# Kernel optimization log

Measured on AMD Instinct MI355X. Metric: run time of the kernel, lower is better.

The kernel has to match this reference:

```python
import jax, jax.numpy as jnp
import numpy as np

IN_F, OUT_F, N_TOK = 4096, 4096, 8192

def setup_inputs() -> dict:
    key = jax.random.key(0)
    k1, k2, k3 = jax.random.split(key, 3)
    x = jax.random.normal(k1, (N_TOK, IN_F), dtype=jnp.float32)
    scaler = jax.random.uniform(k2, (1,), dtype=jnp.float32)
    int8_weights = jax.random.randint(k3, (IN_F, OUT_F), -128, 128, dtype=jnp.int32)
    return {"x": x, "scaler": scaler, "int8_weights": int8_weights}

def reference(x, scaler, int8_weights):
    # dequantize int8 weights: fp_w = int8_w * scaler, then GEMM
    fp_weights = int8_weights.astype(x.dtype) * scaler  # [in, out]
    return jnp.matmul(x, fp_weights)  # [tokens, out]
```

## Files before the change

### kernel.cpp

```cpp
#include <hip/hip_runtime.h>

#define M_DIM 8192
#define N_DIM 4096
#define K_DIM 4096

typedef __attribute__((ext_vector_type(8))) __bf16 bf16x8;
typedef __attribute__((ext_vector_type(4))) float f32x4;
typedef __attribute__((ext_vector_type(8))) unsigned short u16x8;

typedef const __attribute__((address_space(1))) unsigned int gu32_t;
typedef __attribute__((address_space(3))) unsigned int lu32_t;

static __device__ __forceinline__ unsigned short f2bf(float f) {
    union { float f; unsigned int u; } v; v.f = f;
    unsigned int u = v.u;
    return (unsigned short)((u + 0x7fffu + ((u >> 16) & 1u)) >> 16);
}

__global__ __launch_bounds__(256) void cvt_x_kernel(const float* __restrict__ x,
                                                    unsigned short* __restrict__ xb) {
    size_t i = (size_t)blockIdx.x * 256 + threadIdx.x;
    const float4* x4 = (const float4*)x;
    float4 a = x4[2 * i], b = x4[2 * i + 1];
    u16x8 o;
    o[0] = f2bf(a.x); o[1] = f2bf(a.y); o[2] = f2bf(a.z); o[3] = f2bf(a.w);
    o[4] = f2bf(b.x); o[5] = f2bf(b.y); o[6] = f2bf(b.z); o[7] = f2bf(b.w);
    *(u16x8*)(xb + i * 8) = o;
}

__global__ __launch_bounds__(256) void cvt_w_kernel(const int* __restrict__ w,
                                                    unsigned short* __restrict__ wt) {
    __shared__ unsigned short t[64][72];
    int n0 = blockIdx.x * 64;
    int k0 = blockIdx.y * 64;
    int tid = threadIdx.x;
#pragma unroll
    for (int i = 0; i < 16; i++) {
        int idx = tid + i * 256;
        int r = idx >> 6, c = idx & 63;
        int v = w[(size_t)(k0 + r) * N_DIM + n0 + c];
        t[c][r] = f2bf((float)v);
    }
    __syncthreads();
#pragma unroll
    for (int i = 0; i < 2; i++) {
        int slot = tid + i * 256;
        int r = slot >> 3, c = (slot & 7) * 8;
        u16x8 o = *(const u16x8*)&t[r][c];
        *(u16x8*)&wt[(size_t)(n0 + r) * K_DIM + k0 + c] = o;
    }
}

__global__ __launch_bounds__(256) void gemm_bt_kernel(const unsigned short* __restrict__ A,
                                                      const unsigned short* __restrict__ B,
                                                      const float* __restrict__ scaler,
                                                      float* __restrict__ C) {
    __shared__ unsigned short As[128 * 32];
    __shared__ unsigned short Bs[128 * 32];

    const int tid  = threadIdx.x;
    const int m0   = blockIdx.y * 128;
    const int n0   = blockIdx.x * 128;
    const int wave = tid >> 6, lane = tid & 63;
    const int quad = lane >> 4, lr = lane & 15;
    const int wm   = wave >> 1, wn = wave & 1;

    const int q0 = tid, q1 = tid + 256;
    const unsigned short* ga0 = A + (size_t)(m0 + (q0 >> 2)) * K_DIM + (q0 & 3) * 8;
    const unsigned short* ga1 = A + (size_t)(m0 + (q1 >> 2)) * K_DIM + (q1 & 3) * 8;
    const unsigned short* gb0 = B + (size_t)(n0 + (q0 >> 2)) * K_DIM + (q0 & 3) * 8;
    const unsigned short* gb1 = B + (size_t)(n0 + (q1 >> 2)) * K_DIM + (q1 & 3) * 8;
    unsigned short* la0 = As + q0 * 8;
    unsigned short* la1 = As + q1 * 8;
    unsigned short* lb0 = Bs + q0 * 8;
    unsigned short* lb1 = Bs + q1 * 8;

    f32x4 acc[4][4];
#pragma unroll
    for (int i = 0; i < 4; i++)
#pragma unroll
        for (int j = 0; j < 4; j++) acc[i][j] = (f32x4){0.f, 0.f, 0.f, 0.f};

    const unsigned short* pa = &As[(wm * 64 + lr) * 32 + quad * 8];
    const unsigned short* pb = &Bs[(wn * 64 + lr) * 32 + quad * 8];

    for (int kt = 0; kt < K_DIM / 32; ++kt) {
        __builtin_amdgcn_global_load_lds((gu32_t*)ga0, (lu32_t*)la0, 16, 0, 0);
        __builtin_amdgcn_global_load_lds((gu32_t*)ga1, (lu32_t*)la1, 16, 0, 0);
        __builtin_amdgcn_global_load_lds((gu32_t*)gb0, (lu32_t*)lb0, 16, 0, 0);
        __builtin_amdgcn_global_load_lds((gu32_t*)gb1, (lu32_t*)lb1, 16, 0, 0);
        ga0 += 32; ga1 += 32; gb0 += 32; gb1 += 32;
        __syncthreads();

        bf16x8 af[4], bf[4];
#pragma unroll
        for (int mi = 0; mi < 4; mi++) af[mi] = *(const bf16x8*)(pa + mi * 16 * 32);
#pragma unroll
        for (int ni = 0; ni < 4; ni++) bf[ni] = *(const bf16x8*)(pb + ni * 16 * 32);

#pragma unroll
        for (int mi = 0; mi < 4; mi++)
#pragma unroll
            for (int ni = 0; ni < 4; ni++)
                acc[mi][ni] = __builtin_amdgcn_mfma_f32_16x16x32_bf16(
                    af[mi], bf[ni], acc[mi][ni], 0, 0, 0);
        __syncthreads();
    }

    const float s = scaler[0];
#pragma unroll
    for (int mi = 0; mi < 4; mi++)
#pragma unroll
        for (int ni = 0; ni < 4; ni++) {
            const int row = m0 + wm * 64 + mi * 16 + quad * 4;
            const int col = n0 + wn * 64 + ni * 16 + lr;
            float* cp = C + (size_t)row * N_DIM + col;
#pragma unroll
            for (int r = 0; r < 4; r++)
                cp[(size_t)r * N_DIM] = acc[mi][ni][r] * s;
        }
}

extern "C" void kernel_launch(void* const* d_in, const int* in_sizes, int n_in,
                              void* d_out, int out_size, void* d_ws, size_t ws_size,
                              hipStream_t stream) {
    const float* x      = (const float*)d_in[0];
    const float* scaler = (const float*)d_in[1];
    const int*   w      = (const int*)d_in[2];
    float*       out    = (float*)d_out;

    unsigned short* xb = (unsigned short*)d_ws;
    unsigned short* wt = xb + (size_t)M_DIM * K_DIM;

    cvt_x_kernel<<<(M_DIM * (size_t)K_DIM) / (8 * 256), 256, 0, stream>>>(x, xb);
    cvt_w_kernel<<<dim3(N_DIM / 64, K_DIM / 64), 256, 0, stream>>>(w, wt);
    gemm_bt_kernel<<<dim3(N_DIM / 128, M_DIM / 128), 256, 0, stream>>>(xb, wt, scaler, out);
}
```

Before: 575.4 us.

## Switch GEMM to 32x32x16 MFMA tiles and fuse conversion kernels into one launch

The GEMM inner loop now issues 32x32x16 bf16 MFMAs on a 2x2 per-wave tile instead of 16x16x32 on a 4x4 tile. This changes the LDS fragment loads and the output register-to-row mapping. The goal is fewer MFMA issues and LDS reads per k-step. The two preprocessing kernels are also merged into a single launch with a block-index split, which saves one kernel launch; the x conversion now handles 4 floats per thread.

```diff
diff --git a/kernel.cpp b/kernel.cpp
--- a/kernel.cpp
+++ b/kernel.cpp
@@ -5,7 +5,7 @@
 #define K_DIM 4096
 
 typedef __attribute__((ext_vector_type(8))) __bf16 bf16x8;
-typedef __attribute__((ext_vector_type(4))) float f32x4;
+typedef __attribute__((ext_vector_type(16))) float f32x16;
 typedef __attribute__((ext_vector_type(8))) unsigned short u16x8;
 
 typedef const __attribute__((address_space(1))) unsigned int gu32_t;
@@ -17,37 +17,39 @@
     return (unsigned short)((u + 0x7fffu + ((u >> 16) & 1u)) >> 16);
 }
 
-__global__ __launch_bounds__(256) void cvt_x_kernel(const float* __restrict__ x,
-                                                    unsigned short* __restrict__ xb) {
-    size_t i = (size_t)blockIdx.x * 256 + threadIdx.x;
-    const float4* x4 = (const float4*)x;
-    float4 a = x4[2 * i], b = x4[2 * i + 1];
-    u16x8 o;
-    o[0] = f2bf(a.x); o[1] = f2bf(a.y); o[2] = f2bf(a.z); o[3] = f2bf(a.w);
-    o[4] = f2bf(b.x); o[5] = f2bf(b.y); o[6] = f2bf(b.z); o[7] = f2bf(b.w);
-    *(u16x8*)(xb + i * 8) = o;
-}
+#define X_BLOCKS 32768
 
-__global__ __launch_bounds__(256) void cvt_w_kernel(const int* __restrict__ w,
-                                                    unsigned short* __restrict__ wt) {
+__global__ __launch_bounds__(256) void prep_kernel(const float* __restrict__ x,
+                                                   unsigned short* __restrict__ xb,
+                                                   const int* __restrict__ w,
+                                                   unsigned short* __restrict__ wt) {
     __shared__ unsigned short t[64][72];
-    int n0 = blockIdx.x * 64;
-    int k0 = blockIdx.y * 64;
-    int tid = threadIdx.x;
+    const int tid = threadIdx.x;
+    if (blockIdx.x < X_BLOCKS) {
+        size_t g = (size_t)blockIdx.x * 256 + tid;
+        float4 a = ((const float4*)x)[g];
+        ushort4 o;
+        o.x = f2bf(a.x); o.y = f2bf(a.y); o.z = f2bf(a.z); o.w = f2bf(a.w);
+        ((ushort4*)xb)[g] = o;
+    } else {
+        int bid = blockIdx.x - X_BLOCKS;
+        int n0 = (bid & 63) * 64;
+        int k0 = (bid >> 6) * 64;
 #pragma unroll
-    for (int i = 0; i < 16; i++) {
-        int idx = tid + i * 256;
-        int r = idx >> 6, c = idx & 63;
-        int v = w[(size_t)(k0 + r) * N_DIM + n0 + c];
-        t[c][r] = f2bf((float)v);
-    }
-    __syncthreads();
+        for (int i = 0; i < 16; i++) {
+            int idx = tid + i * 256;
+            int r = idx >> 6, c = idx & 63;
+            int v = w[(size_t)(k0 + r) * N_DIM + n0 + c];
+            t[c][r] = f2bf((float)v);
+        }
+        __syncthreads();
 #pragma unroll
-    for (int i = 0; i < 2; i++) {
-        int slot = tid + i * 256;
-        int r = slot >> 3, c = (slot & 7) * 8;
-        u16x8 o = *(const u16x8*)&t[r][c];
-        *(u16x8*)&wt[(size_t)(n0 + r) * K_DIM + k0 + c] = o;
+        for (int i = 0; i < 2; i++) {
+            int slot = tid + i * 256;
+            int r = slot >> 3, c = (slot & 7) * 8;
+            u16x8 o = *(const u16x8*)&t[r][c];
+            *(u16x8*)&wt[(size_t)(n0 + r) * K_DIM + k0 + c] = o;
+        }
     }
 }
 
@@ -62,7 +64,7 @@
     const int m0   = blockIdx.y * 128;
     const int n0   = blockIdx.x * 128;
     const int wave = tid >> 6, lane = tid & 63;
-    const int quad = lane >> 4, lr = lane & 15;
+    const int l31  = lane & 31, lh = lane >> 5;
     const int wm   = wave >> 1, wn = wave & 1;
 
     const int q0 = tid, q1 = tid + 256;
@@ -75,14 +77,16 @@
     unsigned short* lb0 = Bs + q0 * 8;
     unsigned short* lb1 = Bs + q1 * 8;
 
-    f32x4 acc[4][4];
+    f32x16 acc[2][2];
 #pragma unroll
-    for (int i = 0; i < 4; i++)
+    for (int i = 0; i < 2; i++)
 #pragma unroll
-        for (int j = 0; j < 4; j++) acc[i][j] = (f32x4){0.f, 0.f, 0.f, 0.f};
+        for (int j = 0; j < 2; j++)
+#pragma unroll
+            for (int r = 0; r < 16; r++) acc[i][j][r] = 0.f;
 
-    const unsigned short* pa = &As[(wm * 64 + lr) * 32 + quad * 8];
-    const unsigned short* pb = &Bs[(wn * 64 + lr) * 32 + quad * 8];
+    const unsigned short* pa = &As[(wm * 64 + l31) * 32 + lh * 8];
+    const unsigned short* pb = &Bs[(wn * 64 + l31) * 32 + lh * 8];
 
     for (int kt = 0; kt < K_DIM / 32; ++kt) {
         __builtin_amdgcn_global_load_lds((gu32_t*)ga0, (lu32_t*)la0, 16, 0, 0);
@@ -92,32 +96,37 @@
         ga0 += 32; ga1 += 32; gb0 += 32; gb1 += 32;
         __syncthreads();
 
-        bf16x8 af[4], bf[4];
+        bf16x8 af[2][2], bfr[2][2];
 #pragma unroll
-        for (int mi = 0; mi < 4; mi++) af[mi] = *(const bf16x8*)(pa + mi * 16 * 32);
+        for (int ti = 0; ti < 2; ti++)
 #pragma unroll
-        for (int ni = 0; ni < 4; ni++) bf[ni] = *(const bf16x8*)(pb + ni * 16 * 32);
+            for (int ks = 0; ks < 2; ks++) {
+                af[ti][ks]  = *(const bf16x8*)(pa + ti * 32 * 32 + ks * 16);
+                bfr[ti][ks] = *(const bf16x8*)(pb + ti * 32 * 32 + ks * 16);
+            }
 
 #pragma unroll
-        for (int mi = 0; mi < 4; mi++)
+        for (int ks = 0; ks < 2; ks++)
 #pragma unroll
-            for (int ni = 0; ni < 4; ni++)
-                acc[mi][ni] = __builtin_amdgcn_mfma_f32_16x16x32_bf16(
-                    af[mi], bf[ni], acc[mi][ni], 0, 0, 0);
+            for (int ti = 0; ti < 2; ti++)
+#pragma unroll
+                for (int tj = 0; tj < 2; tj++)
+                    acc[ti][tj] = __builtin_amdgcn_mfma_f32_32x32x16_bf16(
+                        af[ti][ks], bfr[tj][ks], acc[ti][tj], 0, 0, 0);
         __syncthreads();
     }
 
     const float s = scaler[0];
 #pragma unroll
-    for (int mi = 0; mi < 4; mi++)
+    for (int ti = 0; ti < 2; ti++)
 #pragma unroll
-        for (int ni = 0; ni < 4; ni++) {
-            const int row = m0 + wm * 64 + mi * 16 + quad * 4;
-            const int col = n0 + wn * 64 + ni * 16 + lr;
-            float* cp = C + (size_t)row * N_DIM + col;
+        for (int tj = 0; tj < 2; tj++) {
+            const int col = n0 + wn * 64 + tj * 32 + l31;
 #pragma unroll
-            for (int r = 0; r < 4; r++)
-                cp[(size_t)r * N_DIM] = acc[mi][ni][r] * s;
+            for (int reg = 0; reg < 16; reg++) {
+                const int row = m0 + wm * 64 + ti * 32 + (reg & 3) + 8 * (reg >> 2) + 4 * lh;
+                C[(size_t)row * N_DIM + col] = acc[ti][tj][reg] * s;
+            }
         }
 }
 
@@ -132,7 +141,6 @@
     unsigned short* xb = (unsigned short*)d_ws;
     unsigned short* wt = xb + (size_t)M_DIM * K_DIM;
 
-    cvt_x_kernel<<<(M_DIM * (size_t)K_DIM) / (8 * 256), 256, 0, stream>>>(x, xb);
-    cvt_w_kernel<<<dim3(N_DIM / 64, K_DIM / 64), 256, 0, stream>>>(w, wt);
+    prep_kernel<<<X_BLOCKS + (N_DIM / 64) * (K_DIM / 64), 256, 0, stream>>>(x, xb, w, wt);
     gemm_bt_kernel<<<dim3(N_DIM / 128, M_DIM / 128), 256, 0, stream>>>(xb, wt, scaler, out);
 }
```

Result: slower. 598.5 us (+4.0%).

## Swizzle LDS tile layout for GEMM and merge conversion kernels into one launch

Applied to the files above, without the earlier changes.

Applies an XOR swizzle to the k-chunk index when staging A and B tiles into LDS via global_load_lds, and applies the matching swizzle on the fragment reads. This is meant to reduce LDS bank conflicts on the 16-byte fragment loads feeding MFMA. It also merges the x and weight conversion kernels into a single launch, with the x part now handling 4 floats per thread. Each global load now reads a permuted 16-byte chunk within its row, and the merged prep kernel reserves LDS even for blocks that only convert x.

```diff
diff --git a/kernel.cpp b/kernel.cpp
--- a/kernel.cpp
+++ b/kernel.cpp
@@ -17,39 +17,43 @@
     return (unsigned short)((u + 0x7fffu + ((u >> 16) & 1u)) >> 16);
 }
 
-__global__ __launch_bounds__(256) void cvt_x_kernel(const float* __restrict__ x,
-                                                    unsigned short* __restrict__ xb) {
-    size_t i = (size_t)blockIdx.x * 256 + threadIdx.x;
-    const float4* x4 = (const float4*)x;
-    float4 a = x4[2 * i], b = x4[2 * i + 1];
-    u16x8 o;
-    o[0] = f2bf(a.x); o[1] = f2bf(a.y); o[2] = f2bf(a.z); o[3] = f2bf(a.w);
-    o[4] = f2bf(b.x); o[5] = f2bf(b.y); o[6] = f2bf(b.z); o[7] = f2bf(b.w);
-    *(u16x8*)(xb + i * 8) = o;
+#define X_BLOCKS 32768
+
+__global__ __launch_bounds__(256) void prep_kernel(const float* __restrict__ x,
+                                                   unsigned short* __restrict__ xb,
+                                                   const int* __restrict__ w,
+                                                   unsigned short* __restrict__ wt) {
+    __shared__ unsigned short t[64][72];
+    const int tid = threadIdx.x;
+    if (blockIdx.x < X_BLOCKS) {
+        size_t g = (size_t)blockIdx.x * 256 + tid;
+        float4 a = ((const float4*)x)[g];
+        ushort4 o;
+        o.x = f2bf(a.x); o.y = f2bf(a.y); o.z = f2bf(a.z); o.w = f2bf(a.w);
+        ((ushort4*)xb)[g] = o;
+    } else {
+        int bid = blockIdx.x - X_BLOCKS;
+        int n0 = (bid & 63) * 64;
+        int k0 = (bid >> 6) * 64;
+#pragma unroll
+        for (int i = 0; i < 16; i++) {
+            int idx = tid + i * 256;
+            int r = idx >> 6, c = idx & 63;
+            int v = w[(size_t)(k0 + r) * N_DIM + n0 + c];
+            t[c][r] = f2bf((float)v);
+        }
+        __syncthreads();
+#pragma unroll
+        for (int i = 0; i < 2; i++) {
+            int slot = tid + i * 256;
+            int r = slot >> 3, c = (slot & 7) * 8;
+            u16x8 o = *(const u16x8*)&t[r][c];
+            *(u16x8*)&wt[(size_t)(n0 + r) * K_DIM + k0 + c] = o;
+        }
+    }
 }
 
-__global__ __launch_bounds__(256) void cvt_w_kernel(const int* __restrict__ w,
-                                                    unsigned short* __restrict__ wt) {
-    __shared__ unsigned short t[64][72];
-    int n0 = blockIdx.x * 64;
-    int k0 = blockIdx.y * 64;
-    int tid = threadIdx.x;
-#pragma unroll
-    for (int i = 0; i < 16; i++) {
-        int idx = tid + i * 256;
-        int r = idx >> 6, c = idx & 63;
-        int v = w[(size_t)(k0 + r) * N_DIM + n0 + c];
-        t[c][r] = f2bf((float)v);
-    }
-    __syncthreads();
-#pragma unroll
-    for (int i = 0; i < 2; i++) {
-        int slot = tid + i * 256;
-        int r = slot >> 3, c = (slot & 7) * 8;
-        u16x8 o = *(const u16x8*)&t[r][c];
-        *(u16x8*)&wt[(size_t)(n0 + r) * K_DIM + k0 + c] = o;
-    }
-}
+static __device__ __forceinline__ int swz(int m) { return (m + (m >> 2)) & 3; }
 
 __global__ __launch_bounds__(256) void gemm_bt_kernel(const unsigned short* __restrict__ A,
                                                       const unsigned short* __restrict__ B,
@@ -66,10 +70,12 @@
     const int wm   = wave >> 1, wn = wave & 1;
 
     const int q0 = tid, q1 = tid + 256;
-    const unsigned short* ga0 = A + (size_t)(m0 + (q0 >> 2)) * K_DIM + (q0 & 3) * 8;
-    const unsigned short* ga1 = A + (size_t)(m0 + (q1 >> 2)) * K_DIM + (q1 & 3) * 8;
-    const unsigned short* gb0 = B + (size_t)(n0 + (q0 >> 2)) * K_DIM + (q0 & 3) * 8;
-    const unsigned short* gb1 = B + (size_t)(n0 + (q1 >> 2)) * K_DIM + (q1 & 3) * 8;
+    const int r0 = q0 >> 2, kc0 = (q0 & 3) ^ swz(r0);
+    const int r1 = q1 >> 2, kc1 = (q1 & 3) ^ swz(r1);
+    const unsigned short* ga0 = A + (size_t)(m0 + r0) * K_DIM + kc0 * 8;
+    const unsigned short* ga1 = A + (size_t)(m0 + r1) * K_DIM + kc1 * 8;
+    const unsigned short* gb0 = B + (size_t)(n0 + r0) * K_DIM + kc0 * 8;
+    const unsigned short* gb1 = B + (size_t)(n0 + r1) * K_DIM + kc1 * 8;
     unsigned short* la0 = As + q0 * 8;
     unsigned short* la1 = As + q1 * 8;
     unsigned short* lb0 = Bs + q0 * 8;
@@ -81,8 +87,10 @@
 #pragma unroll
         for (int j = 0; j < 4; j++) acc[i][j] = (f32x4){0.f, 0.f, 0.f, 0.f};
 
-    const unsigned short* pa = &As[(wm * 64 + lr) * 32 + quad * 8];
-    const unsigned short* pb = &Bs[(wn * 64 + lr) * 32 + quad * 8];
+    const int swa = quad ^ swz(wm * 64 + lr);
+    const int swb = quad ^ swz(wn * 64 + lr);
+    const unsigned short* pa = &As[((wm * 64 + lr) * 4 + swa) * 8];
+    const unsigned short* pb = &Bs[((wn * 64 + lr) * 4 + swb) * 8];
 
     for (int kt = 0; kt < K_DIM / 32; ++kt) {
         __builtin_amdgcn_global_load_lds((gu32_t*)ga0, (lu32_t*)la0, 16, 0, 0);
@@ -94,9 +102,9 @@
 
         bf16x8 af[4], bf[4];
 #pragma unroll
-        for (int mi = 0; mi < 4; mi++) af[mi] = *(const bf16x8*)(pa + mi * 16 * 32);
+        for (int mi = 0; mi < 4; mi++) af[mi] = *(const bf16x8*)(pa + mi * 512);
 #pragma unroll
-        for (int ni = 0; ni < 4; ni++) bf[ni] = *(const bf16x8*)(pb + ni * 16 * 32);
+        for (int ni = 0; ni < 4; ni++) bf[ni] = *(const bf16x8*)(pb + ni * 512);
 
 #pragma unroll
         for (int mi = 0; mi < 4; mi++)
@@ -132,7 +140,6 @@
     unsigned short* xb = (unsigned short*)d_ws;
     unsigned short* wt = xb + (size_t)M_DIM * K_DIM;
 
-    cvt_x_kernel<<<(M_DIM * (size_t)K_DIM) / (8 * 256), 256, 0, stream>>>(x, xb);
-    cvt_w_kernel<<<dim3(N_DIM / 64, K_DIM / 64), 256, 0, stream>>>(w, wt);
+    prep_kernel<<<X_BLOCKS + (N_DIM / 64) * (K_DIM / 64), 256, 0, stream>>>(x, xb, w, wt);
     gemm_bt_kernel<<<dim3(N_DIM / 128, M_DIM / 128), 256, 0, stream>>>(xb, wt, scaler, out);
 }
```

Result: faster. 560.8 us (-2.5%).
